# Kernel optimization log

Measured on AMD Instinct MI355X. Metric: run time of the kernel, lower is better.

Reference implementation:

```python
import jax, jax.numpy as jnp
import numpy as np

B, NX, NC, D, H = 2, 512, 4096, 1024, 16
HD = D // H  # head_dim = context_dim // heads
LN_EPS = 1e-5


def setup_inputs() -> dict:
    key = jax.random.key(0)
    k0, k1, k2, k3, k4 = jax.random.split(key, 5)
    x = jax.random.normal(k0, (B, NX, D), dtype=jnp.float32)
    c = jax.random.normal(k1, (B, NC, D), dtype=jnp.float32)
    attn_mask = jax.random.randint(k2, (B, NX, NC), 0, 2).astype(bool)
    # learned params
    ln_w = jnp.ones((D,), jnp.float32)
    ln_b = jnp.zeros((D,), jnp.float32)
    Wq = jax.random.normal(k3, (D, D), dtype=jnp.float32) * 0.02  # to_q (query_dim -> inner_dim)
    Wo = jax.random.normal(k4, (D, D), dtype=jnp.float32) * 0.02  # to_out (inner_dim -> query_dim)
    return {"x": x, "c": c, "attn_mask": attn_mask, "ln_w": ln_w, "ln_b": ln_b, "Wq": Wq, "Wo": Wo}


def _layernorm(x, w, b):
    mu = jnp.mean(x, axis=-1, keepdims=True)
    var = jnp.mean(jnp.square(x - mu), axis=-1, keepdims=True)
    return (x - mu) * jax.lax.rsqrt(var + LN_EPS) * w + b


def reference(x, c, attn_mask, ln_w, ln_b, Wq, Wo):
    scale = HD ** (-0.5)
    xn = _layernorm(x, ln_w, ln_b)
    q = (xn @ Wq).reshape(B, NX, H, HD).transpose(0, 2, 1, 3)      # (B,H,NX,HD)
    kv0 = c.reshape(B, NC, H, HD).transpose(0, 2, 1, 3)             # (B,H,NC,HD) -- kvt=(kv0,kv0)
    kv = jnp.concatenate([q, kv0], axis=2)                          # kv_append_q=True -> (B,H,NX+NC,HD)
    # mask: ones for the appended-q block, user mask for context block
    m = jnp.broadcast_to(attn_mask[:, None, :, :], (B, H, NX, NC))
    full_mask = jnp.concatenate([jnp.ones((B, H, NX, NX), bool), m], axis=-1)
    sim = jnp.einsum('bhqd,bhkd->bhqk', q * scale, kv)              # (B,H,NX,NX+NC)
    neg = -jnp.finfo(sim.dtype).max
    sim = jnp.where(full_mask, sim, neg)
    attn = jax.nn.softmax(sim, axis=-1)
    a = jnp.einsum('bhqk,bhkd->bhqd', attn, kv)
    o = a.transpose(0, 2, 1, 3).reshape(B, NX, H * HD) @ Wo
    return (o, kv0)
```

## Files before the change

### kernel.cpp

```cpp
#include <hip/hip_runtime.h>

#define B_  2
#define NX_ 512
#define NC_ 4096
#define D_  1024
#define H_  16
#define HD_ 64
#define NT_ (NX_ + NC_)
#define NSPLIT 6
#define KBS (NT_ / 64 / NSPLIT)

typedef float  floatx4  __attribute__((ext_vector_type(4)));
typedef __bf16 bf16x8   __attribute__((ext_vector_type(8)));
typedef unsigned short ushort8v __attribute__((ext_vector_type(8)));

__device__ __forceinline__ bf16x8 as_bf16x8(ushort8v u) {
    union { ushort8v u; bf16x8 b; } c; c.u = u; return c.b;
}
__device__ __forceinline__ unsigned short f2bf(float f) {
    unsigned u = __float_as_uint(f);
    u += 0x7FFF + ((u >> 16) & 1);
    return (unsigned short)(u >> 16);
}

__global__ __launch_bounds__(256)
void prep_kernel(const float* __restrict__ x, const float* __restrict__ lw,
                 const float* __restrict__ lb, const float* __restrict__ Wq,
                 const float* __restrict__ Wo, const int* __restrict__ mask,
                 const float* __restrict__ c,
                 unsigned short* __restrict__ xnb, unsigned short* __restrict__ WqT,
                 unsigned short* __restrict__ WoT, unsigned* __restrict__ bits,
                 unsigned short* __restrict__ cbf, float* __restrict__ gz,
                 float* __restrict__ kv0o) {
    int blk = blockIdx.x;
    int tid = threadIdx.x;
    if (blk < 1024) {
        int row = blk;
        float4 v = reinterpret_cast<const float4*>(x)[(size_t)row * (D_ / 4) + tid];
        float s  = v.x + v.y + v.z + v.w;
        float s2 = v.x * v.x + v.y * v.y + v.z * v.z + v.w * v.w;
        #pragma unroll
        for (int off = 32; off > 0; off >>= 1) {
            s  += __shfl_down(s, off);
            s2 += __shfl_down(s2, off);
        }
        __shared__ float sm[4], sm2[4], stat[2];
        int wv = tid >> 6;
        if ((tid & 63) == 0) { sm[wv] = s; sm2[wv] = s2; }
        __syncthreads();
        if (tid == 0) {
            float S  = sm[0] + sm[1] + sm[2] + sm[3];
            float S2 = sm2[0] + sm2[1] + sm2[2] + sm2[3];
            float mu  = S * (1.0f / D_);
            float var = fmaxf(S2 * (1.0f / D_) - mu * mu, 0.0f);
            stat[0] = mu;
            stat[1] = rsqrtf(var + 1e-5f);
        }
        __syncthreads();
        float mu = stat[0], rs = stat[1];
        float4 w4 = reinterpret_cast<const float4*>(lw)[tid];
        float4 b4 = reinterpret_cast<const float4*>(lb)[tid];
        ushort4 o;
        o.x = f2bf((v.x - mu) * rs * w4.x + b4.x);
        o.y = f2bf((v.y - mu) * rs * w4.y + b4.y);
        o.z = f2bf((v.z - mu) * rs * w4.z + b4.z);
        o.w = f2bf((v.w - mu) * rs * w4.w + b4.w);
        reinterpret_cast<ushort4*>(xnb)[(size_t)row * (D_ / 4) + tid] = o;
    } else if (blk < 1536) {
        int which = (blk - 1024) >> 8;
        int t = (blk - 1024) & 255;
        const float* W = which ? Wo : Wq;
        unsigned short* WT = which ? WoT : WqT;
        __shared__ unsigned short T[64][72];
        int row0 = (t >> 4) * 64, col0 = (t & 15) * 64;
        int r = tid >> 2, ch = (tid & 3) * 16;
        const float* src = W + (size_t)(row0 + r) * D_ + col0 + ch;
        unsigned short vals[16];
        #pragma unroll
        for (int k = 0; k < 4; ++k) {
            float4 v = reinterpret_cast<const float4*>(src)[k];
            vals[k*4+0] = f2bf(v.x); vals[k*4+1] = f2bf(v.y);
            vals[k*4+2] = f2bf(v.z); vals[k*4+3] = f2bf(v.w);
        }
        #pragma unroll
        for (int i = 0; i < 16; ++i) T[ch + i][r] = vals[i];
        __syncthreads();
        unsigned short* dst = WT + (size_t)(col0 + r) * D_ + row0 + ch;
        uint4 o0 = *reinterpret_cast<uint4*>(&T[r][ch]);
        uint4 o1 = *reinterpret_cast<uint4*>(&T[r][ch + 8]);
        *reinterpret_cast<uint4*>(dst)     = o0;
        *reinterpret_cast<uint4*>(dst + 8) = o1;
    } else if (blk < 2048) {
        size_t w = (size_t)(blk - 1536) * 256 + tid;
        const int* src = mask + w * 32;
        unsigned b = 0;
        #pragma unroll
        for (int k = 0; k < 8; ++k) {
            int4 v = reinterpret_cast<const int4*>(src)[k];
            b |= (v.x != 0 ? 1u : 0u) << (k * 4 + 0);
            b |= (v.y != 0 ? 1u : 0u) << (k * 4 + 1);
            b |= (v.z != 0 ? 1u : 0u) << (k * 4 + 2);
            b |= (v.w != 0 ? 1u : 0u) << (k * 4 + 3);
        }
        bits[w] = b;
    } else if (blk < 10240) {
        size_t i = ((size_t)(blk - 2048) * 256 + tid) * 4;
        float4 v = *reinterpret_cast<const float4*>(c + i);
        ushort4 o;
        o.x = f2bf(v.x); o.y = f2bf(v.y); o.z = f2bf(v.z); o.w = f2bf(v.w);
        *reinterpret_cast<ushort4*>(cbf + i) = o;
        if (kv0o != nullptr) {
            size_t row = i >> 10;
            int dd = (int)(i & 1023);
            int hh = dd >> 6, d4 = (dd & 63) >> 2;
            int bb = (int)(row >> 12);
            int n  = (int)(row & 4095);
            size_t o4 = (((size_t)(bb * 16 + hh) * NC_ + n) << 4) + d4;
            reinterpret_cast<float4*>(kv0o)[o4] = v;
        }
    } else {
        size_t i = ((size_t)(blk - 10240) * 256 + tid) * 4;
        float4 z = {0.f, 0.f, 0.f, 0.f};
        *reinterpret_cast<float4*>(gz + i) = z;
    }
}

__global__ __launch_bounds__(256)
void kv0_kernel(const float* __restrict__ c, float* __restrict__ out2) {
    size_t i = (size_t)blockIdx.x * 256 + threadIdx.x;
    int d4 = (int)(i & 15);
    size_t r = i >> 4;
    int n = (int)(r % NC_);
    size_t r2 = r / NC_;
    int h = (int)(r2 & (H_ - 1));
    int b = (int)(r2 >> 4);
    float4 v = *reinterpret_cast<const float4*>(c + ((size_t)(b * NC_ + n)) * D_ + h * HD_ + d4 * 4);
    reinterpret_cast<float4*>(out2)[i] = v;
}

__global__ __launch_bounds__(256)
void gemm_bt_kernel(const unsigned short* __restrict__ A, const unsigned short* __restrict__ BT,
                    unsigned short* __restrict__ Cb) {
    __shared__ unsigned short As[64][72];
    __shared__ unsigned short Bs[64][72];
    int tid = threadIdx.x;
    int lane = tid & 63, wave = tid >> 6;
    int m16 = lane & 15, g = lane >> 4, g8 = g * 8;
    int row0 = blockIdx.y * 64, col0 = blockIdx.x * 64;
    int r = tid >> 2, ch = (tid & 3) * 16;

    floatx4 acc[4];
    #pragma unroll
    for (int t = 0; t < 4; ++t) acc[t] = (floatx4){0.f, 0.f, 0.f, 0.f};

    for (int kc = 0; kc < 16; ++kc) {
        int k0 = kc * 64;
        const unsigned short* asrc = A  + (size_t)(row0 + r) * D_ + k0 + ch;
        const unsigned short* bsrc = BT + (size_t)(col0 + r) * D_ + k0 + ch;
        uint4 a0 = *reinterpret_cast<const uint4*>(asrc);
        uint4 a1 = *reinterpret_cast<const uint4*>(asrc + 8);
        uint4 b0 = *reinterpret_cast<const uint4*>(bsrc);
        uint4 b1 = *reinterpret_cast<const uint4*>(bsrc + 8);
        *reinterpret_cast<uint4*>(&As[r][ch])     = a0;
        *reinterpret_cast<uint4*>(&As[r][ch + 8]) = a1;
        *reinterpret_cast<uint4*>(&Bs[r][ch])     = b0;
        *reinterpret_cast<uint4*>(&Bs[r][ch + 8]) = b1;
        __syncthreads();
        bf16x8 fa0 = as_bf16x8(*reinterpret_cast<ushort8v*>(&As[16 * wave + m16][g8]));
        bf16x8 fa1 = as_bf16x8(*reinterpret_cast<ushort8v*>(&As[16 * wave + m16][32 + g8]));
        #pragma unroll
        for (int t = 0; t < 4; ++t) {
            bf16x8 fb0 = as_bf16x8(*reinterpret_cast<ushort8v*>(&Bs[16 * t + m16][g8]));
            bf16x8 fb1 = as_bf16x8(*reinterpret_cast<ushort8v*>(&Bs[16 * t + m16][32 + g8]));
            acc[t] = __builtin_amdgcn_mfma_f32_16x16x32_bf16(fa0, fb0, acc[t], 0, 0, 0);
            acc[t] = __builtin_amdgcn_mfma_f32_16x16x32_bf16(fa1, fb1, acc[t], 0, 0, 0);
        }
        __syncthreads();
    }
    #pragma unroll
    for (int t = 0; t < 4; ++t)
        #pragma unroll
        for (int reg = 0; reg < 4; ++reg)
            Cb[(size_t)(row0 + 16 * wave + g * 4 + reg) * D_ + col0 + 16 * t + m16] = f2bf(acc[t][reg]);
}

__global__ __launch_bounds__(256)
void gemm_attn_kernel(const float* __restrict__ gacc, const float* __restrict__ gacc_l,
                      const unsigned short* __restrict__ BT, float* __restrict__ out) {
    __shared__ unsigned short As[64][72];
    __shared__ unsigned short Bs[64][72];
    int tid = threadIdx.x;
    int lane = tid & 63, wave = tid >> 6;
    int m16 = lane & 15, g = lane >> 4, g8 = g * 8;
    int row0 = blockIdx.y * 64, col0 = blockIdx.x * 64;
    int r = tid >> 2, ch = (tid & 3) * 16;

    floatx4 acc[4];
    #pragma unroll
    for (int t = 0; t < 4; ++t) acc[t] = (floatx4){0.f, 0.f, 0.f, 0.f};

    for (int kc = 0; kc < 16; ++kc) {
        int k0 = kc * 64;
        int row = row0 + r;
        float inv = 1.0f / fmaxf(gacc_l[(size_t)row * H_ + kc], 1e-35f);
        const float* asrc = gacc + (size_t)row * D_ + k0 + ch;
        const unsigned short* bsrc = BT + (size_t)(col0 + r) * D_ + k0 + ch;
        unsigned short av[16];
        #pragma unroll
        for (int t = 0; t < 4; ++t) {
            float4 v = reinterpret_cast<const float4*>(asrc)[t];
            av[t*4+0] = f2bf(v.x * inv); av[t*4+1] = f2bf(v.y * inv);
            av[t*4+2] = f2bf(v.z * inv); av[t*4+3] = f2bf(v.w * inv);
        }
        uint4 b0 = *reinterpret_cast<const uint4*>(bsrc);
        uint4 b1 = *reinterpret_cast<const uint4*>(bsrc + 8);
        *reinterpret_cast<uint4*>(&As[r][ch])     = *reinterpret_cast<uint4*>(&av[0]);
        *reinterpret_cast<uint4*>(&As[r][ch + 8]) = *reinterpret_cast<uint4*>(&av[8]);
        *reinterpret_cast<uint4*>(&Bs[r][ch])     = b0;
        *reinterpret_cast<uint4*>(&Bs[r][ch + 8]) = b1;
        __syncthreads();
        bf16x8 fa0 = as_bf16x8(*reinterpret_cast<ushort8v*>(&As[16 * wave + m16][g8]));
        bf16x8 fa1 = as_bf16x8(*reinterpret_cast<ushort8v*>(&As[16 * wave + m16][32 + g8]));
        #pragma unroll
        for (int t = 0; t < 4; ++t) {
            bf16x8 fb0 = as_bf16x8(*reinterpret_cast<ushort8v*>(&Bs[16 * t + m16][g8]));
            bf16x8 fb1 = as_bf16x8(*reinterpret_cast<ushort8v*>(&Bs[16 * t + m16][32 + g8]));
            acc[t] = __builtin_amdgcn_mfma_f32_16x16x32_bf16(fa0, fb0, acc[t], 0, 0, 0);
            acc[t] = __builtin_amdgcn_mfma_f32_16x16x32_bf16(fa1, fb1, acc[t], 0, 0, 0);
        }
        __syncthreads();
    }
    #pragma unroll
    for (int t = 0; t < 4; ++t)
        #pragma unroll
        for (int reg = 0; reg < 4; ++reg)
            out[(size_t)(row0 + 16 * wave + g * 4 + reg) * D_ + col0 + 16 * t + m16] = acc[t][reg];
}

__global__ __launch_bounds__(256, 6)
void attn_kernel(const unsigned short* __restrict__ qbf,
                 const unsigned short* __restrict__ cbf,
                 const unsigned* __restrict__ maskbits,
                 float* __restrict__ gacc, float* __restrict__ gacc_l) {
    int blk   = blockIdx.x;
    int xcd   = blk & 7;
    int rest  = blk >> 3;
    int grp   = rest / 48;
    int inner = rest - grp * 48;
    int bh    = grp * 8 + xcd;
    int qt    = inner & 7;
    int split = inner >> 3;
    int h  = bh & 15;
    int b  = bh >> 4;
    int tid  = threadIdx.x;
    int lane = tid & 63;
    int wave = tid >> 6;
    int m16  = lane & 15;
    int g    = lane >> 4;
    int g8   = g * 8;

    __shared__ unsigned short Ks [64][72];
    __shared__ unsigned short Kts[64][72];
    __shared__ unsigned short Ps [64][64];

    const unsigned short* qrow = qbf + ((size_t)(b * NX_ + qt * 64 + 16 * wave + m16)) * D_ + h * HD_;
    bf16x8 qa0 = as_bf16x8(*reinterpret_cast<const ushort8v*>(qrow + g8));
    bf16x8 qa1 = as_bf16x8(*reinterpret_cast<const ushort8v*>(qrow + 32 + g8));

    floatx4 acc_o[4];
    #pragma unroll
    for (int td = 0; td < 4; ++td) acc_o[td] = (floatx4){0.f, 0.f, 0.f, 0.f};
    floatx4 acc_l = (floatx4){0.f, 0.f, 0.f, 0.f};

    ushort8v ones_u;
    #pragma unroll
    for (int j = 0; j < 8; ++j) ones_u[j] = 0x3F80;
    bf16x8 onesf = as_bf16x8(ones_u);

    int Kg = tid >> 4;
    int Dg = tid & 15;
    int pcst = ((Kg >> 1) + (Dg >> 1)) & 7;
    int prsw = 2 * ((m16 >> 2) & 3);

    int kb0 = split * KBS;

    uint2 rows[4];
    {
        const unsigned short* s0 = (kb0 < 8)
            ? qbf + ((size_t)(b * NX_ + kb0 * 64 + 4 * Kg)) * D_ + h * HD_ + 4 * Dg
            : cbf + ((size_t)(b * NC_ + kb0 * 64 - NX_ + 4 * Kg)) * D_ + h * HD_ + 4 * Dg;
        #pragma unroll
        for (int kk = 0; kk < 4; ++kk)
            rows[kk] = *reinterpret_cast<const uint2*>(s0 + (size_t)kk * D_);
    }

    for (int i = 0; i < KBS; ++i) {
        int kb = kb0 + i;
        __syncthreads();

        unsigned mw0[4], mw1[4];
        if (kb >= 8) {
            #pragma unroll
            for (int r = 0; r < 4; ++r) {
                size_t mi = ((size_t)(b * NX_ + qt * 64 + 16 * wave + g * 4 + r)) * (NC_ / 32)
                          + (size_t)(kb - 8) * 2;
                uint2 w = *reinterpret_cast<const uint2*>(&maskbits[mi]);
                mw0[r] = w.x; mw1[r] = w.y;
            }
        }

        #pragma unroll
        for (int kk = 0; kk < 4; ++kk)
            *reinterpret_cast<uint2*>(&Ks[4 * Kg + kk][4 * Dg]) = rows[kk];
        #pragma unroll
        for (int i2 = 0; i2 < 4; ++i2) {
            unsigned sel = (i2 & 1) ? 0x07060302u : 0x05040100u;
            unsigned r0 = (i2 >> 1) ? rows[0].y : rows[0].x;
            unsigned r1 = (i2 >> 1) ? rows[1].y : rows[1].x;
            unsigned r2 = (i2 >> 1) ? rows[2].y : rows[2].x;
            unsigned r3 = (i2 >> 1) ? rows[3].y : rows[3].x;
            uint2 cw;
            cw.x = __builtin_amdgcn_perm(r1, r0, sel);
            cw.y = __builtin_amdgcn_perm(r3, r2, sel);
            *reinterpret_cast<uint2*>(&Kts[4 * Dg + i2][pcst * 8 + 4 * (Kg & 1)]) = cw;
        }

        {
            int kbn = (i + 1 < KBS) ? kb + 1 : kb;
            const unsigned short* sn = (kbn < 8)
                ? qbf + ((size_t)(b * NX_ + kbn * 64 + 4 * Kg)) * D_ + h * HD_ + 4 * Dg
                : cbf + ((size_t)(b * NC_ + kbn * 64 - NX_ + 4 * Kg)) * D_ + h * HD_ + 4 * Dg;
            #pragma unroll
            for (int kk = 0; kk < 4; ++kk)
                rows[kk] = *reinterpret_cast<const uint2*>(sn + (size_t)kk * D_);
        }

        asm volatile("s_waitcnt lgkmcnt(0)" ::: "memory");
        __builtin_amdgcn_s_barrier();
        __builtin_amdgcn_sched_barrier(0);
        asm volatile("" ::: "memory");

        floatx4 accs[4];
        #pragma unroll
        for (int t = 0; t < 4; ++t) {
            bf16x8 b0 = as_bf16x8(*reinterpret_cast<ushort8v*>(&Ks[16 * t + m16][g8]));
            bf16x8 b1 = as_bf16x8(*reinterpret_cast<ushort8v*>(&Ks[16 * t + m16][32 + g8]));
            floatx4 d = (floatx4){0.f, 0.f, 0.f, 0.f};
            d = __builtin_amdgcn_mfma_f32_16x16x32_bf16(qa0, b0, d, 0, 0, 0);
            d = __builtin_amdgcn_mfma_f32_16x16x32_bf16(qa1, b1, d, 0, 0, 0);
            accs[t] = d;
        }

        const float C1 = 0.18033688011112042f;
        const float C2 = 92.33248261689366f;
        #pragma unroll
        for (int t = 0; t < 4; ++t) {
            int cc = 2 * t + (m16 >> 3);
            #pragma unroll
            for (int r = 0; r < 4; ++r) {
                float e = fminf(fmaf(accs[t][r], C1, -C2), 0.0f);
                float p = __builtin_amdgcn_exp2f(e);
                if (kb >= 8) {
                    unsigned w = (t < 2) ? mw0[r] : mw1[r];
                    unsigned bit = (w >> ((16 * t + m16) & 31)) & 1u;
                    p = bit ? p : 0.0f;
                }
                int prow = 16 * wave + g * 4 + r;
                int pc = (cc + 2 * g) & 7;
                Ps[prow][pc * 8 + (m16 & 7)] = (unsigned short)(__float_as_uint(p) >> 16);
            }
        }
        asm volatile("s_waitcnt lgkmcnt(0)" ::: "memory");

        bf16x8 p0 = as_bf16x8(*reinterpret_cast<ushort8v*>(&Ps[16 * wave + m16][((g + prsw) & 7) * 8]));
        bf16x8 p1 = as_bf16x8(*reinterpret_cast<ushort8v*>(&Ps[16 * wave + m16][((4 + g + prsw) & 7) * 8]));
        acc_l = __builtin_amdgcn_mfma_f32_16x16x32_bf16(p0, onesf, acc_l, 0, 0, 0);
        acc_l = __builtin_amdgcn_mfma_f32_16x16x32_bf16(p1, onesf, acc_l, 0, 0, 0);
        #pragma unroll
        for (int td = 0; td < 4; ++td) {
            int row = 16 * td + m16;
            int rh = row >> 3;
            bf16x8 v0 = as_bf16x8(*reinterpret_cast<ushort8v*>(&Kts[row][((g + rh) & 7) * 8]));
            bf16x8 v1 = as_bf16x8(*reinterpret_cast<ushort8v*>(&Kts[row][((4 + g + rh) & 7) * 8]));
            acc_o[td] = __builtin_amdgcn_mfma_f32_16x16x32_bf16(p0, v0, acc_o[td], 0, 0, 0);
            acc_o[td] = __builtin_amdgcn_mfma_f32_16x16x32_bf16(p1, v1, acc_o[td], 0, 0, 0);
        }
    }

    #pragma unroll
    for (int r = 0; r < 4; ++r) {
        int qrow_ = qt * 64 + 16 * wave + g * 4 + r;
        float* dst = gacc + ((size_t)(b * NX_ + qrow_)) * D_ + h * HD_;
        #pragma unroll
        for (int td = 0; td < 4; ++td)
            unsafeAtomicAdd(&dst[16 * td + m16], acc_o[td][r]);
        if (m16 == 0)
            unsafeAtomicAdd(&gacc_l[(size_t)(b * NX_ + qrow_) * H_ + h], acc_l[r]);
    }
}

extern "C" void kernel_launch(void* const* d_in, const int* in_sizes, int n_in,
                              void* d_out, int out_size, void* d_ws, size_t ws_size,
                              hipStream_t stream) {
    (void)in_sizes; (void)n_in; (void)out_size;
    const float* x    = (const float*)d_in[0];
    const float* c    = (const float*)d_in[1];
    const int*   mask = (const int*)d_in[2];
    const float* ln_w = (const float*)d_in[3];
    const float* ln_b = (const float*)d_in[4];
    const float* Wq   = (const float*)d_in[5];
    const float* Wo   = (const float*)d_in[6];
    float* out  = (float*)d_out;
    float* out2 = out + (size_t)B_ * NX_ * D_;

    const size_t SCRATCH_FLOATS = 8011776;
    bool use_ws = (d_ws != nullptr) && (ws_size >= SCRATCH_FLOATS * sizeof(float));
    float* base = use_ws ? (float*)d_ws : out2;

    unsigned short* qbf      = (unsigned short*)(base);
    unsigned*       maskbits = (unsigned*)(base + 524288);
    float*          gacc     = base + 655360;
    float*          gacc_l   = base + 1703936;
    unsigned short* WqT      = (unsigned short*)(base + 1720320);
    unsigned short* WoT      = (unsigned short*)(base + 2244608);
    unsigned short* xnb      = (unsigned short*)(base + 2768896);
    unsigned short* cbf      = (unsigned short*)(base + 3817472);

    prep_kernel<<<11280, 256, 0, stream>>>(x, ln_w, ln_b, Wq, Wo, mask, c,
                                           xnb, WqT, WoT, maskbits, cbf, gacc,
                                           use_ws ? out2 : nullptr);
    gemm_bt_kernel<<<dim3(16, 16), 256, 0, stream>>>(xnb, WqT, qbf);
    attn_kernel<<<NSPLIT * 256, 256, 0, stream>>>(qbf, cbf, maskbits, gacc, gacc_l);
    gemm_attn_kernel<<<dim3(16, 16), 256, 0, stream>>>(gacc, gacc_l, WoT, out);
    if (!use_ws)
        kv0_kernel<<<(B_ * H_ * NC_ * HD_ / 4) / 256, 256, 0, stream>>>(c, out2);
}
```

Baseline: 223.3 us.

## Prefetch GEMM tiles into registers, reduce attention splits, add MFMA priority hints

Both projection GEMMs now load the next k-chunk from global memory into registers while the current chunk is computed, and the trailing barrier is replaced by a single leading barrier with explicit waitcnt. The attention kernel drops from six to four key splits, with matching occupancy bounds and simpler block-to-head indexing. It also raises wave priority around its MFMA sections and swaps __syncthreads for a raw barrier. Fewer splits mean fewer atomic partial-sum writes but fewer blocks to fill the GPU. The register prefetch adds register pressure.

Measured after the change: 182.5 us. 1.22x faster.

```diff
diff --git a/kernel.cpp b/kernel.cpp
--- a/kernel.cpp
+++ b/kernel.cpp
@@ -7,7 +7,7 @@
 #define H_  16
 #define HD_ 64
 #define NT_ (NX_ + NC_)
-#define NSPLIT 6
+#define NSPLIT 4
 #define KBS (NT_ / 64 / NSPLIT)
 
 typedef float  floatx4  __attribute__((ext_vector_type(4)));
@@ -153,19 +153,31 @@
     #pragma unroll
     for (int t = 0; t < 4; ++t) acc[t] = (floatx4){0.f, 0.f, 0.f, 0.f};
 
+    const unsigned short* abase = A  + (size_t)(row0 + r) * D_ + ch;
+    const unsigned short* bbase = BT + (size_t)(col0 + r) * D_ + ch;
+    uint4 a0 = *reinterpret_cast<const uint4*>(abase);
+    uint4 a1 = *reinterpret_cast<const uint4*>(abase + 8);
+    uint4 b0 = *reinterpret_cast<const uint4*>(bbase);
+    uint4 b1 = *reinterpret_cast<const uint4*>(bbase + 8);
+
     for (int kc = 0; kc < 16; ++kc) {
-        int k0 = kc * 64;
-        const unsigned short* asrc = A  + (size_t)(row0 + r) * D_ + k0 + ch;
-        const unsigned short* bsrc = BT + (size_t)(col0 + r) * D_ + k0 + ch;
-        uint4 a0 = *reinterpret_cast<const uint4*>(asrc);
-        uint4 a1 = *reinterpret_cast<const uint4*>(asrc + 8);
-        uint4 b0 = *reinterpret_cast<const uint4*>(bsrc);
-        uint4 b1 = *reinterpret_cast<const uint4*>(bsrc + 8);
+        if (kc) {
+            asm volatile("s_waitcnt lgkmcnt(0)" ::: "memory");
+            __builtin_amdgcn_s_barrier();
+        }
         *reinterpret_cast<uint4*>(&As[r][ch])     = a0;
         *reinterpret_cast<uint4*>(&As[r][ch + 8]) = a1;
         *reinterpret_cast<uint4*>(&Bs[r][ch])     = b0;
         *reinterpret_cast<uint4*>(&Bs[r][ch + 8]) = b1;
-        __syncthreads();
+        if (kc < 15) {
+            int k0 = (kc + 1) * 64;
+            a0 = *reinterpret_cast<const uint4*>(abase + k0);
+            a1 = *reinterpret_cast<const uint4*>(abase + k0 + 8);
+            b0 = *reinterpret_cast<const uint4*>(bbase + k0);
+            b1 = *reinterpret_cast<const uint4*>(bbase + k0 + 8);
+        }
+        asm volatile("s_waitcnt lgkmcnt(0)" ::: "memory");
+        __builtin_amdgcn_s_barrier();
         bf16x8 fa0 = as_bf16x8(*reinterpret_cast<ushort8v*>(&As[16 * wave + m16][g8]));
         bf16x8 fa1 = as_bf16x8(*reinterpret_cast<ushort8v*>(&As[16 * wave + m16][32 + g8]));
         #pragma unroll
@@ -175,7 +187,6 @@
             acc[t] = __builtin_amdgcn_mfma_f32_16x16x32_bf16(fa0, fb0, acc[t], 0, 0, 0);
             acc[t] = __builtin_amdgcn_mfma_f32_16x16x32_bf16(fa1, fb1, acc[t], 0, 0, 0);
         }
-        __syncthreads();
     }
     #pragma unroll
     for (int t = 0; t < 4; ++t)
@@ -194,31 +205,47 @@
     int m16 = lane & 15, g = lane >> 4, g8 = g * 8;
     int row0 = blockIdx.y * 64, col0 = blockIdx.x * 64;
     int r = tid >> 2, ch = (tid & 3) * 16;
+    int row = row0 + r;
 
     floatx4 acc[4];
     #pragma unroll
     for (int t = 0; t < 4; ++t) acc[t] = (floatx4){0.f, 0.f, 0.f, 0.f};
 
+    const float* abase = gacc + (size_t)row * D_ + ch;
+    const unsigned short* bbase = BT + (size_t)(col0 + r) * D_ + ch;
+    float4 av4[4];
+    uint4 b0, b1;
+    float inv = 1.0f / fmaxf(gacc_l[(size_t)row * H_ + 0], 1e-35f);
+    #pragma unroll
+    for (int t = 0; t < 4; ++t) av4[t] = reinterpret_cast<const float4*>(abase)[t];
+    b0 = *reinterpret_cast<const uint4*>(bbase);
+    b1 = *reinterpret_cast<const uint4*>(bbase + 8);
+
     for (int kc = 0; kc < 16; ++kc) {
-        int k0 = kc * 64;
-        int row = row0 + r;
-        float inv = 1.0f / fmaxf(gacc_l[(size_t)row * H_ + kc], 1e-35f);
-        const float* asrc = gacc + (size_t)row * D_ + k0 + ch;
-        const unsigned short* bsrc = BT + (size_t)(col0 + r) * D_ + k0 + ch;
+        if (kc) {
+            asm volatile("s_waitcnt lgkmcnt(0)" ::: "memory");
+            __builtin_amdgcn_s_barrier();
+        }
         unsigned short av[16];
         #pragma unroll
         for (int t = 0; t < 4; ++t) {
-            float4 v = reinterpret_cast<const float4*>(asrc)[t];
-            av[t*4+0] = f2bf(v.x * inv); av[t*4+1] = f2bf(v.y * inv);
-            av[t*4+2] = f2bf(v.z * inv); av[t*4+3] = f2bf(v.w * inv);
-        }
-        uint4 b0 = *reinterpret_cast<const uint4*>(bsrc);
-        uint4 b1 = *reinterpret_cast<const uint4*>(bsrc + 8);
+            av[t*4+0] = f2bf(av4[t].x * inv); av[t*4+1] = f2bf(av4[t].y * inv);
+            av[t*4+2] = f2bf(av4[t].z * inv); av[t*4+3] = f2bf(av4[t].w * inv);
+        }
         *reinterpret_cast<uint4*>(&As[r][ch])     = *reinterpret_cast<uint4*>(&av[0]);
         *reinterpret_cast<uint4*>(&As[r][ch + 8]) = *reinterpret_cast<uint4*>(&av[8]);
         *reinterpret_cast<uint4*>(&Bs[r][ch])     = b0;
         *reinterpret_cast<uint4*>(&Bs[r][ch + 8]) = b1;
-        __syncthreads();
+        if (kc < 15) {
+            int k0 = (kc + 1) * 64;
+            inv = 1.0f / fmaxf(gacc_l[(size_t)row * H_ + kc + 1], 1e-35f);
+            #pragma unroll
+            for (int t = 0; t < 4; ++t) av4[t] = reinterpret_cast<const float4*>(abase + k0)[t];
+            b0 = *reinterpret_cast<const uint4*>(bbase + k0);
+            b1 = *reinterpret_cast<const uint4*>(bbase + k0 + 8);
+        }
+        asm volatile("s_waitcnt lgkmcnt(0)" ::: "memory");
+        __builtin_amdgcn_s_barrier();
         bf16x8 fa0 = as_bf16x8(*reinterpret_cast<ushort8v*>(&As[16 * wave + m16][g8]));
         bf16x8 fa1 = as_bf16x8(*reinterpret_cast<ushort8v*>(&As[16 * wave + m16][32 + g8]));
         #pragma unroll
@@ -228,7 +255,6 @@
             acc[t] = __builtin_amdgcn_mfma_f32_16x16x32_bf16(fa0, fb0, acc[t], 0, 0, 0);
             acc[t] = __builtin_amdgcn_mfma_f32_16x16x32_bf16(fa1, fb1, acc[t], 0, 0, 0);
         }
-        __syncthreads();
     }
     #pragma unroll
     for (int t = 0; t < 4; ++t)
@@ -237,17 +263,14 @@
             out[(size_t)(row0 + 16 * wave + g * 4 + reg) * D_ + col0 + 16 * t + m16] = acc[t][reg];
 }
 
-__global__ __launch_bounds__(256, 6)
+__global__ __launch_bounds__(256, 4)
 void attn_kernel(const unsigned short* __restrict__ qbf,
                  const unsigned short* __restrict__ cbf,
                  const unsigned* __restrict__ maskbits,
                  float* __restrict__ gacc, float* __restrict__ gacc_l) {
     int blk   = blockIdx.x;
-    int xcd   = blk & 7;
-    int rest  = blk >> 3;
-    int grp   = rest / 48;
-    int inner = rest - grp * 48;
-    int bh    = grp * 8 + xcd;
+    int bh    = ((blk >> 8) << 3) | (blk & 7);
+    int inner = (blk >> 3) & 31;
     int qt    = inner & 7;
     int split = inner >> 3;
     int h  = bh & 15;
@@ -296,7 +319,8 @@
 
     for (int i = 0; i < KBS; ++i) {
         int kb = kb0 + i;
-        __syncthreads();
+        asm volatile("s_waitcnt lgkmcnt(0)" ::: "memory");
+        __builtin_amdgcn_s_barrier();
 
         unsigned mw0[4], mw1[4];
         if (kb >= 8) {
@@ -341,6 +365,7 @@
         asm volatile("" ::: "memory");
 
         floatx4 accs[4];
+        __builtin_amdgcn_s_setprio(1);
         #pragma unroll
         for (int t = 0; t < 4; ++t) {
             bf16x8 b0 = as_bf16x8(*reinterpret_cast<ushort8v*>(&Ks[16 * t + m16][g8]));
@@ -350,6 +375,7 @@
             d = __builtin_amdgcn_mfma_f32_16x16x32_bf16(qa1, b1, d, 0, 0, 0);
             accs[t] = d;
         }
+        __builtin_amdgcn_s_setprio(0);
 
         const float C1 = 0.18033688011112042f;
         const float C2 = 92.33248261689366f;
@@ -374,6 +400,7 @@
 
         bf16x8 p0 = as_bf16x8(*reinterpret_cast<ushort8v*>(&Ps[16 * wave + m16][((g + prsw) & 7) * 8]));
         bf16x8 p1 = as_bf16x8(*reinterpret_cast<ushort8v*>(&Ps[16 * wave + m16][((4 + g + prsw) & 7) * 8]));
+        __builtin_amdgcn_s_setprio(1);
         acc_l = __builtin_amdgcn_mfma_f32_16x16x32_bf16(p0, onesf, acc_l, 0, 0, 0);
         acc_l = __builtin_amdgcn_mfma_f32_16x16x32_bf16(p1, onesf, acc_l, 0, 0, 0);
         #pragma unroll
@@ -385,6 +412,7 @@
             acc_o[td] = __builtin_amdgcn_mfma_f32_16x16x32_bf16(p0, v0, acc_o[td], 0, 0, 0);
             acc_o[td] = __builtin_amdgcn_mfma_f32_16x16x32_bf16(p1, v1, acc_o[td], 0, 0, 0);
         }
+        __builtin_amdgcn_s_setprio(0);
     }
 
     #pragma unroll
```
